# Performance work log

Hardware: AMD Instinct MI355X
Metric: run time of the kernel (lower is better)

Reference implementation:

```python
import jax, jax.numpy as jnp
import numpy as np
from jax import lax

HIDDEN = 1024
OUT = 256
BATCH = 1024
SEQ_LEN = 128


def setup_inputs() -> dict:
    key = jax.random.key(0)
    ks = jax.random.split(key, 7)
    s_ih = 1.0 / np.sqrt(HIDDEN)
    # PyTorch GRUCell params: weight_ih [3H, I], weight_hh [3H, H], biases [3H]
    W_ih = jax.random.uniform(ks[0], (3 * HIDDEN, OUT), jnp.float32, -s_ih, s_ih)
    W_hh = jax.random.uniform(ks[1], (3 * HIDDEN, HIDDEN), jnp.float32, -s_ih, s_ih)
    b_ih = jax.random.uniform(ks[2], (3 * HIDDEN,), jnp.float32, -s_ih, s_ih)
    b_hh = jax.random.uniform(ks[3], (3 * HIDDEN,), jnp.float32, -s_ih, s_ih)
    # xavier_uniform Linear(hidden -> out), bias zero
    lim = float(np.sqrt(2.0) * np.sqrt(6.0 / (HIDDEN + OUT)))
    W_dec = jax.random.uniform(ks[4], (OUT, HIDDEN), jnp.float32, -lim, lim)
    b_dec = jnp.zeros((OUT,), jnp.float32)
    h_0 = jax.random.normal(ks[5], (1, BATCH, HIDDEN), jnp.float32)
    return {
        "h_0": h_0,
        "W_ih": W_ih,
        "W_hh": W_hh,
        "b_ih": b_ih,
        "b_hh": b_hh,
        "W_dec": W_dec,
        "b_dec": b_dec,
        "seq_len": SEQ_LEN,
    }


def _gru_cell(x, h, W_ih, W_hh, b_ih, b_hh):
    # PyTorch GRUCell math
    gi = x @ W_ih.T + b_ih  # [B, 3H]
    gh = h @ W_hh.T + b_hh  # [B, 3H]
    i_r, i_z, i_n = jnp.split(gi, 3, axis=-1)
    h_r, h_z, h_n = jnp.split(gh, 3, axis=-1)
    r = jax.nn.sigmoid(i_r + h_r)
    z = jax.nn.sigmoid(i_z + h_z)
    n = jnp.tanh(i_n + r * h_n)
    return (1.0 - z) * n + z * h


def reference(h_0, W_ih, W_hh, b_ih, b_hh, W_dec, b_dec, seq_len):
    h = h_0[0]  # squeeze(0) -> [B, H]
    x = h @ W_dec.T + b_dec  # initial x_i [B, OUT]

    def step(carry, _):
        h, x = carry
        h_new = _gru_cell(x, h, W_ih, W_hh, b_ih, b_hh)
        x_new = h_new @ W_dec.T + b_dec
        return (h_new, x_new), x_new

    _, xs = lax.scan(step, (h, x), None, length=seq_len)  # [T, B, OUT]
    return jnp.transpose(xs, (1, 0, 2))  # [B, T, OUT]
```

## Files before the change

### kernel.cpp

```cpp
#include <hip/hip_runtime.h>
#include <cstdint>
#include <cstddef>


#define HD 1024
#define OD 256
#define TS 128
#define NBUF 4
#define ABUF 16384
#define BBUF 18432

typedef _Float16 f16x8 __attribute__((ext_vector_type(8)));
typedef float f32x4 __attribute__((ext_vector_type(4)));

template <int AUX>
__device__ __forceinline__ void gl_lds16(const void* g, void* l) {
  auto gp = reinterpret_cast<const __attribute__((address_space(1))) unsigned int*>(
      reinterpret_cast<uintptr_t>(g));
  auto lp = reinterpret_cast<__attribute__((address_space(3))) unsigned int*>(
      reinterpret_cast<uintptr_t>(l));
  __builtin_amdgcn_global_load_lds(gp, lp, 16, 0, AUX);
}

__device__ __forceinline__ void st_h16_dev(_Float16* p, _Float16 v) {
  asm volatile("global_store_short %0, %1, off sc0 sc1"
               :: "v"(p), "v"(v) : "memory");
}

__global__ __launch_bounds__(256) void prep_w(
    const float* __restrict__ Wih,
    const float* __restrict__ Whh,
    const float* __restrict__ Wdec,
    _Float16* __restrict__ Wws)
{
  int blk = blockIdx.x, tid = threadIdx.x;
  int k0 = tid * 4;
  if (blk < 768) {
    int cbv[4], rrv[4], jg[4], jh[4];
    #pragma unroll
    for (int rsel = 0; rsel < 4; ++rsel) {
      int dj = blk * 4 + rsel;
      int cb = dj / 96, rr = dj % 96;
      int s = rr >> 5, wcol = (rr >> 4) & 1, p = rr & 15;
      int j = cb * 32 + wcol * 16 + p;
      cbv[rsel] = cb; rrv[rsel] = rr;
      jg[rsel] = s * 1024 + j;
      jh[rsel] = (s == 0) ? j : (s == 1 ? 1024 + j : -1);
    }
    float acc[4][4];
    #pragma unroll
    for (int a = 0; a < 4; ++a) { acc[a][0]=0.f; acc[a][1]=0.f; acc[a][2]=0.f; acc[a][3]=0.f; }
    for (int q = 0; q < 256; ++q) {
      float4 wd = *(const float4*)(Wdec + (size_t)q * 1024 + k0);
      #pragma unroll
      for (int a = 0; a < 4; ++a) {
        float w = Wih[(size_t)jg[a] * 256 + q];
        acc[a][0] += w * wd.x; acc[a][1] += w * wd.y;
        acc[a][2] += w * wd.z; acc[a][3] += w * wd.w;
      }
    }
    #pragma unroll
    for (int a = 0; a < 4; ++a) {
      if (jh[a] >= 0) {
        const float* wh = Whh + (size_t)jh[a] * 1024 + k0;
        acc[a][0] += wh[0]; acc[a][1] += wh[1];
        acc[a][2] += wh[2]; acc[a][3] += wh[3];
      }
      _Float16* dst = Wws + ((size_t)cbv[a] * 144 + rrv[a]) * 1024 + k0;
      dst[0] = (_Float16)acc[a][0]; dst[1] = (_Float16)acc[a][1];
      dst[2] = (_Float16)acc[a][2]; dst[3] = (_Float16)acc[a][3];
    }
  } else {
    #pragma unroll
    for (int rsel = 0; rsel < 4; ++rsel) {
      int cr = (blk - 768) * 4 + rsel;
      int cb = cr / 48, rr = 96 + cr % 48;
      _Float16* dst = Wws + ((size_t)cb * 144 + rr) * 1024 + k0;
      if (rr < 128) {
        int j = cb * 32 + ((rr >> 4) & 1) * 16 + (rr & 15);
        const float* src = Whh + (size_t)(2048 + j) * 1024 + k0;
        dst[0] = (_Float16)src[0]; dst[1] = (_Float16)src[1];
        dst[2] = (_Float16)src[2]; dst[3] = (_Float16)src[3];
      } else if (rr < 136) {
        const float* src = Wdec + (size_t)(cb * 8 + rr - 128) * 1024 + k0;
        dst[0] = (_Float16)src[0]; dst[1] = (_Float16)src[1];
        dst[2] = (_Float16)src[2]; dst[3] = (_Float16)src[3];
      } else {
        dst[0] = (_Float16)0.f; dst[1] = (_Float16)0.f;
        dst[2] = (_Float16)0.f; dst[3] = (_Float16)0.f;
      }
    }
  }
}

__global__ __launch_bounds__(256) void prep_bias(
    const float* __restrict__ Wih,
    const float* __restrict__ bih, const float* __restrict__ bhh,
    const float* __restrict__ bdec_in,
    float* __restrict__ br, float* __restrict__ bz, float* __restrict__ bin_,
    float* __restrict__ bhn, float* __restrict__ bdec,
    unsigned int* __restrict__ ctr)
{
  int j = blockIdx.x * 256 + threadIdx.x;
  if (blockIdx.x == 0) ctr[threadIdx.x] = 0u;
  float bc0 = 0.f, bc1 = 0.f, bc2 = 0.f;
  for (int q = 0; q < 256; ++q) {
    float bd = bdec_in[q];
    bc0 += Wih[(size_t)j * 256 + q] * bd;
    bc1 += Wih[(size_t)(1024 + j) * 256 + q] * bd;
    bc2 += Wih[(size_t)(2048 + j) * 256 + q] * bd;
  }
  br[j]  = bih[j]        + bhh[j]        + bc0;
  bz[j]  = bih[1024 + j] + bhh[1024 + j] + bc1;
  bin_[j]= bih[2048 + j] + bc2;
  bhn[j] = bhh[2048 + j];
  if (j < 256) bdec[j] = bdec_in[j];
}

__global__ __launch_bounds__(256) void prep_h(
    const float* __restrict__ h0, _Float16* __restrict__ h16)
{
  int i = blockIdx.x * 256 + threadIdx.x;
  h16[i] = (_Float16)h0[i];
}

__global__ __launch_bounds__(256, 1) void fused_gru(
    const _Float16* __restrict__ Wws,
    const float* __restrict__ br, const float* __restrict__ bz,
    const float* __restrict__ bin_, const float* __restrict__ bhn,
    const float* __restrict__ bdec,
    const float* __restrict__ h0,
    _Float16* __restrict__ h16A, _Float16* __restrict__ h16B,
    float* __restrict__ out,
    unsigned int* __restrict__ ctr)
{
  __shared__ __align__(16) char lds[NBUF * (ABUF + BBUF)];

  const int tid = threadIdx.x;
  const int wave = tid >> 6, lane = tid & 63;
  const int mt = blockIdx.x >> 5, cb = blockIdx.x & 31;
  const int wr = wave >> 1, wc = wave & 1;
  const int col16 = lane & 15, quad = lane >> 4;

  const _Float16* __restrict__ slab = Wws + (size_t)cb * (144 * 1024);

  int offs[4];
  #pragma unroll
  for (int jj = 0; jj < 4; ++jj) {
    int m = (wave * 4 + jj) * 64 + lane;
    int r = m >> 3, c = m & 7, g = c ^ (r & 7);
    offs[jj] = r * 1024 + g * 8;
  }
  int offE;
  { int m = 1024 + tid; int r = m >> 3, c = m & 7, g = c ^ (r & 7);
    offE = r * 1024 + g * 8; }

  const int swz = (quad ^ (col16 & 7)) << 4;

  const int j = cb * 32 + wc * 16 + col16;
  const float vbr = br[j], vbz = bz[j], vbi = bin_[j], vbh = bhn[j];
  const float vb = bdec[cb * 8 + (col16 & 7)];

  float hold[4][4];
  #pragma unroll
  for (int fm = 0; fm < 4; ++fm) {
    const int mbase = mt * 128 + 64 * wr + 16 * fm + quad * 4;
    #pragma unroll
    for (int ri = 0; ri < 4; ++ri)
      hold[fm][ri] = h0[(size_t)(mbase + ri) * 1024 + j];
  }
  asm volatile("s_waitcnt vmcnt(0)" ::: "memory");

  auto issue_B = [&](int bsel, int kc) {
    char* Bb = lds + NBUF * ABUF + bsel * BBUF;
    #pragma unroll
    for (int jj = 0; jj < 4; ++jj)
      gl_lds16<0>(slab + offs[jj] + kc, Bb + (wave * 4 + jj) * 1024);
    if (wave < 2)
      gl_lds16<0>(slab + offE + kc, Bb + 16384 + wave * 1024);
  };

  const f32x4 fzero = {0.f, 0.f, 0.f, 0.f};

  issue_B(0, 0);
  issue_B(1, 64);
  issue_B(2, 128);

  #pragma unroll 1
  for (int t = 0; t <= TS; ++t) {
    const _Float16* __restrict__ Abase =
        ((t & 1) ? h16B : h16A) + (size_t)mt * (128 * 1024);
    _Float16* __restrict__ o16 = (t & 1) ? h16A : h16B;

    auto issue_A = [&](int bsel, int kc) {
      char* Ab = lds + bsel * ABUF;
      #pragma unroll
      for (int jj = 0; jj < 4; ++jj)
        gl_lds16<17>(Abase + offs[jj] + kc, Ab + (wave * 4 + jj) * 1024);
    };
    auto issue_set = [&](int bsel, int kc) {
      char* Ab = lds + bsel * ABUF;
      char* Bb = lds + NBUF * ABUF + bsel * BBUF;
      #pragma unroll
      for (int jj = 0; jj < 4; ++jj) {
        gl_lds16<17>(Abase + offs[jj] + kc, Ab + (wave * 4 + jj) * 1024);
        gl_lds16<0>(slab  + offs[jj] + kc, Bb + (wave * 4 + jj) * 1024);
      }
      if (wave < 2)
        gl_lds16<0>(slab + offE + kc, Bb + 16384 + wave * 1024);
    };

    f32x4 accG[4][4]; f32x4 accD[2];
    #pragma unroll
    for (int i = 0; i < 4; ++i)
      #pragma unroll
      for (int jj = 0; jj < 4; ++jj) accG[i][jj] = fzero;
    accD[0] = fzero; accD[1] = fzero;

    issue_A(0, 0);
    issue_A(1, 64);
    issue_A(2, 128);

    #pragma unroll 1
    for (int ki = 0; ki < 16; ++ki) {
      const int cur = ki & 3;
      __builtin_amdgcn_sched_barrier(0);
      if (ki == 0) {
        asm volatile("s_waitcnt vmcnt(8)" ::: "memory");
      } else if (ki == 1) {
        if (wave < 2) asm volatile("s_waitcnt vmcnt(13)" ::: "memory");
        else          asm volatile("s_waitcnt vmcnt(12)" ::: "memory");
      } else if (ki <= 13) {
        if (wave < 2) asm volatile("s_waitcnt vmcnt(18)" ::: "memory");
        else          asm volatile("s_waitcnt vmcnt(16)" ::: "memory");
      } else if (ki == 14) {
        if (wave < 2) asm volatile("s_waitcnt vmcnt(9)" ::: "memory");
        else          asm volatile("s_waitcnt vmcnt(8)" ::: "memory");
      } else {
        asm volatile("s_waitcnt vmcnt(0)" ::: "memory");
      }
      __builtin_amdgcn_s_barrier();
      __builtin_amdgcn_sched_barrier(0);

      if (ki <= 12) issue_set((ki + 3) & 3, (ki + 3) * 64);

      const char* As = lds + cur * ABUF;
      const char* Bs = lds + NBUF * ABUF + cur * BBUF;

      #pragma unroll
      for (int half = 0; half < 2; ++half) {
        const int sz = swz ^ (half << 6);
        f16x8 af[4], bg[4], bdv;
        #pragma unroll
        for (int fm = 0; fm < 4; ++fm)
          af[fm] = *(const f16x8*)(As + (64 * wr + 16 * fm + col16) * 128 + sz);
        #pragma unroll
        for (int fn = 0; fn < 4; ++fn)
          bg[fn] = *(const f16x8*)(Bs + (32 * fn + wc * 16 + col16) * 128 + sz);
        bdv = *(const f16x8*)(Bs + (128 + col16) * 128 + sz);
        const f16x8 adv0 = wc ? af[2] : af[0];
        const f16x8 adv1 = wc ? af[3] : af[1];

        __builtin_amdgcn_s_setprio(1);
        #pragma unroll
        for (int fm = 0; fm < 4; ++fm)
          #pragma unroll
          for (int fn = 0; fn < 4; ++fn)
            accG[fm][fn] = __builtin_amdgcn_mfma_f32_16x16x32_f16(af[fm], bg[fn], accG[fm][fn], 0, 0, 0);
        accD[0] = __builtin_amdgcn_mfma_f32_16x16x32_f16(adv0, bdv, accD[0], 0, 0, 0);
        accD[1] = __builtin_amdgcn_mfma_f32_16x16x32_f16(adv1, bdv, accD[1], 0, 0, 0);
        __builtin_amdgcn_s_setprio(0);
      }
    }

    if (t < TS) {
      #pragma unroll
      for (int fm = 0; fm < 4; ++fm) {
        const int mbase = mt * 128 + 64 * wr + 16 * fm + quad * 4;
        #pragma unroll
        for (int ri = 0; ri < 4; ++ri) {
          const int m = mbase + ri;
          float rg = 1.f / (1.f + __expf(-(accG[fm][0][ri] + vbr)));
          float zg = 1.f / (1.f + __expf(-(accG[fm][1][ri] + vbz)));
          float nn = tanhf(accG[fm][2][ri] + vbi + rg * (accG[fm][3][ri] + vbh));
          float hnew = (1.f - zg) * nn + zg * hold[fm][ri];
          hold[fm][ri] = hnew;
          st_h16_dev(o16 + (size_t)m * 1024 + j, (_Float16)hnew);
        }
      }
    }
    if (t > 0 && col16 < 8) {
      const int oc = cb * 8 + col16;
      #pragma unroll
      for (int d = 0; d < 2; ++d) {
        const int mbase = mt * 128 + 32 * wave + 16 * d + quad * 4;
        #pragma unroll
        for (int ri = 0; ri < 4; ++ri) {
          const int m = mbase + ri;
          out[(size_t)m * (TS * OD) + (size_t)(t - 1) * OD + oc] = accD[d][ri] + vb;
        }
      }
    }

    if (t < TS) {
      __syncthreads();
      issue_B(0, 0);
      issue_B(1, 64);
      issue_B(2, 128);
      if (tid == 0) {
        __hip_atomic_fetch_add(&ctr[mt * 32], 1u, __ATOMIC_RELAXED, __HIP_MEMORY_SCOPE_AGENT);
        while (__hip_atomic_load(&ctr[mt * 32], __ATOMIC_RELAXED, __HIP_MEMORY_SCOPE_AGENT)
               < 32u * (unsigned)(t + 1)) {
          __builtin_amdgcn_s_sleep(1);
        }
      }
      __builtin_amdgcn_s_barrier();
      __builtin_amdgcn_sched_barrier(0);
    }
  }
}

__global__ __launch_bounds__(256, 1) void step_kernel(
    const _Float16* __restrict__ Wws,
    const float* __restrict__ br, const float* __restrict__ bz,
    const float* __restrict__ bin_, const float* __restrict__ bhn,
    const float* __restrict__ bdec,
    const _Float16* __restrict__ h_in16, const float* __restrict__ h_in32,
    _Float16* __restrict__ h_out16, float* __restrict__ h_out32,
    float* __restrict__ out, int t)
{
  __shared__ __align__(16) char lds[2 * 16384 + 2 * 18432];

  const int tid = threadIdx.x;
  const int wave = tid >> 6, lane = tid & 63;
  const int mt = blockIdx.x >> 5, cb = blockIdx.x & 31;
  const int wr = wave >> 1, wc = wave & 1;
  const int col16 = lane & 15, quad = lane >> 4;

  const _Float16* __restrict__ slab  = Wws + (size_t)cb * (144 * 1024);
  const _Float16* __restrict__ Abase = h_in16 + (size_t)mt * (128 * 1024);

  int offs[4];
  #pragma unroll
  for (int jj = 0; jj < 4; ++jj) {
    int m = (wave * 4 + jj) * 64 + lane;
    int r = m >> 3, c = m & 7, g = c ^ (r & 7);
    offs[jj] = r * 1024 + g * 8;
  }
  int offE;
  { int m = 1024 + tid; int r = m >> 3, c = m & 7, g = c ^ (r & 7);
    offE = r * 1024 + g * 8; }

  const int swz = (quad ^ (col16 & 7)) << 4;

  f32x4 accG[4][4]; f32x4 accD[2];
  const f32x4 fzero = {0.f, 0.f, 0.f, 0.f};
  #pragma unroll
  for (int i = 0; i < 4; ++i)
    #pragma unroll
    for (int jj = 0; jj < 4; ++jj) accG[i][jj] = fzero;
  accD[0] = fzero; accD[1] = fzero;

  auto issue_dma = [&](int bsel, int kc) {
    char* Ab = lds + bsel * 16384;
    char* Bb = lds + 32768 + bsel * 18432;
    #pragma unroll
    for (int jj = 0; jj < 4; ++jj) {
      gl_lds16<0>(Abase + offs[jj] + kc, Ab + (wave * 4 + jj) * 1024);
      gl_lds16<0>(slab  + offs[jj] + kc, Bb + (wave * 4 + jj) * 1024);
    }
    if (wave < 2)
      gl_lds16<0>(slab + offE + kc, Bb + 16384 + wave * 1024);
  };

  issue_dma(0, 0);
  __syncthreads();

  #pragma unroll 1
  for (int ki = 0; ki < 16; ++ki) {
    const int cur = ki & 1;
    if (ki < 15) issue_dma(cur ^ 1, (ki + 1) * 64);
    const char* As = lds + cur * 16384;
    const char* Bs = lds + 32768 + cur * 18432;

    #pragma unroll
    for (int half = 0; half < 2; ++half) {
      const int sz = swz ^ (half << 6);
      f16x8 af[4], bg[4], bdv;
      #pragma unroll
      for (int fm = 0; fm < 4; ++fm)
        af[fm] = *(const f16x8*)(As + (64 * wr + 16 * fm + col16) * 128 + sz);
      #pragma unroll
      for (int fn = 0; fn < 4; ++fn)
        bg[fn] = *(const f16x8*)(Bs + (32 * fn + wc * 16 + col16) * 128 + sz);
      bdv = *(const f16x8*)(Bs + (128 + col16) * 128 + sz);
      const f16x8 adv0 = wc ? af[2] : af[0];
      const f16x8 adv1 = wc ? af[3] : af[1];

      #pragma unroll
      for (int fm = 0; fm < 4; ++fm)
        #pragma unroll
        for (int fn = 0; fn < 4; ++fn)
          accG[fm][fn] = __builtin_amdgcn_mfma_f32_16x16x32_f16(af[fm], bg[fn], accG[fm][fn], 0, 0, 0);
      accD[0] = __builtin_amdgcn_mfma_f32_16x16x32_f16(adv0, bdv, accD[0], 0, 0, 0);
      accD[1] = __builtin_amdgcn_mfma_f32_16x16x32_f16(adv1, bdv, accD[1], 0, 0, 0);
    }
    __syncthreads();
  }

  if (t < TS) {
    const int jj2 = cb * 32 + wc * 16 + col16;
    const float vbr = br[jj2], vbz = bz[jj2], vbi = bin_[jj2], vbh = bhn[jj2];
    #pragma unroll
    for (int fm = 0; fm < 4; ++fm) {
      const int mbase = mt * 128 + 64 * wr + 16 * fm + quad * 4;
      #pragma unroll
      for (int ri = 0; ri < 4; ++ri) {
        const int m = mbase + ri;
        float rg = 1.f / (1.f + __expf(-(accG[fm][0][ri] + vbr)));
        float zg = 1.f / (1.f + __expf(-(accG[fm][1][ri] + vbz)));
        float nn = tanhf(accG[fm][2][ri] + vbi + rg * (accG[fm][3][ri] + vbh));
        float hold = h_in32[(size_t)m * 1024 + jj2];
        float hnew = (1.f - zg) * nn + zg * hold;
        h_out32[(size_t)m * 1024 + jj2] = hnew;
        h_out16[(size_t)m * 1024 + jj2] = (_Float16)hnew;
      }
    }
  }
  if (t > 0 && col16 < 8) {
    const int oc = cb * 8 + col16;
    const float vb = bdec[oc];
    #pragma unroll
    for (int d = 0; d < 2; ++d) {
      const int mbase = mt * 128 + 32 * wave + 16 * d + quad * 4;
      #pragma unroll
      for (int ri = 0; ri < 4; ++ri) {
        const int m = mbase + ri;
        out[(size_t)m * (TS * OD) + (size_t)(t - 1) * OD + oc] = accD[d][ri] + vb;
      }
    }
  }
}

extern "C" void kernel_launch(void* const* d_in, const int* in_sizes, int n_in,
                              void* d_out, int out_size, void* d_ws, size_t ws_size,
                              hipStream_t stream) {
  const float* h0      = (const float*)d_in[0];
  const float* Wih     = (const float*)d_in[1];
  const float* Whh     = (const float*)d_in[2];
  const float* bih     = (const float*)d_in[3];
  const float* bhh     = (const float*)d_in[4];
  const float* Wdec    = (const float*)d_in[5];
  const float* bdec_in = (const float*)d_in[6];
  float* out = (float*)d_out;

  char* ws = (char*)d_ws;
  _Float16* Wws = (_Float16*)ws;
  float* br   = (float*)(ws + 9437184);
  float* bz   = (float*)(ws + 9437184 + 4096);
  float* bin_ = (float*)(ws + 9437184 + 8192);
  float* bhn  = (float*)(ws + 9437184 + 12288);
  float* bdec = (float*)(ws + 9437184 + 16384);
  _Float16* h16A = (_Float16*)(ws + 9461760);
  _Float16* h16B = h16A + 1024 * 1024;
  unsigned int* ctr = (unsigned int*)(ws + 9461760 + 4194304);
  float* h32A = (float*)(ws + 9461760 + 4194304 + 4096);
  float* h32B = h32A + 1024 * 1024;

  prep_w<<<1152, 256, 0, stream>>>(Wih, Whh, Wdec, Wws);
  prep_bias<<<4, 256, 0, stream>>>(Wih, bih, bhh, bdec_in, br, bz, bin_, bhn, bdec, ctr);
  prep_h<<<4096, 256, 0, stream>>>(h0, h16A);

  void* kargs[] = {
    (void*)&Wws, (void*)&br, (void*)&bz, (void*)&bin_, (void*)&bhn, (void*)&bdec,
    (void*)&h0, (void*)&h16A, (void*)&h16B, (void*)&out, (void*)&ctr
  };
  hipError_t cerr = hipLaunchCooperativeKernel((void*)fused_gru, dim3(256), dim3(256),
                                               kargs, 0, stream);
  if (cerr != hipSuccess) {
    for (int t = 0; t <= TS; ++t) {
      const _Float16* in16 = (t & 1) ? h16B : h16A;
      const float*    in32 = (t == 0) ? h0 : ((t & 1) ? h32B : h32A);
      _Float16*       o16  = (t & 1) ? h16A : h16B;
      float*          o32  = (t & 1) ? h32A : h32B;
      step_kernel<<<256, 256, 0, stream>>>(Wws, br, bz, bin_, bhn, bdec,
                                           in16, in32, o16, o32, out, t);
    }
  }
}
```

Measured before the change: 2.582 ms.

## Split K across two wave groups in fused GRU kernel with LDS reduction

Doubles the persistent block to 512 threads: two groups of four waves each compute half of the K dimension, each with its own double-buffered A/B staging, and then exchange partial accumulators through LDS to reduce before the gate epilogue. Each group handles half of the epilogue rows, and the weight prefetch for the next step is issued before the epilogue. The intent is more waves per CU to hide load latency on the latency-bound recurrent step, at the cost of an extra LDS reduction, extra barriers, and a shallower pipeline (2 buffers per group instead of 4). tanhf is also replaced with an exp-based fast tanh.

```diff
diff --git a/kernel.cpp b/kernel.cpp
--- a/kernel.cpp
+++ b/kernel.cpp
@@ -6,7 +6,6 @@
 #define HD 1024
 #define OD 256
 #define TS 128
-#define NBUF 4
 #define ABUF 16384
 #define BBUF 18432
 
@@ -25,6 +24,10 @@
 __device__ __forceinline__ void st_h16_dev(_Float16* p, _Float16 v) {
   asm volatile("global_store_short %0, %1, off sc0 sc1"
                :: "v"(p), "v"(v) : "memory");
+}
+
+__device__ __forceinline__ float fast_tanh(float x) {
+  return 1.f - 2.f / (__expf(2.f * x) + 1.f);
 }
 
 __global__ __launch_bounds__(256) void prep_w(
@@ -124,7 +127,7 @@
   h16[i] = (_Float16)h0[i];
 }
 
-__global__ __launch_bounds__(256, 1) void fused_gru(
+__global__ __launch_bounds__(512, 2) void fused_gru(
     const _Float16* __restrict__ Wws,
     const float* __restrict__ br, const float* __restrict__ bz,
     const float* __restrict__ bin_, const float* __restrict__ bhn,
@@ -134,12 +137,13 @@
     float* __restrict__ out,
     unsigned int* __restrict__ ctr)
 {
-  __shared__ __align__(16) char lds[NBUF * (ABUF + BBUF)];
+  __shared__ __align__(16) char lds[4 * (ABUF + BBUF) + 8192];
 
   const int tid = threadIdx.x;
   const int wave = tid >> 6, lane = tid & 63;
+  const int s = wave >> 2, p = wave & 3;
   const int mt = blockIdx.x >> 5, cb = blockIdx.x & 31;
-  const int wr = wave >> 1, wc = wave & 1;
+  const int wr = p >> 1, wc = p & 1;
   const int col16 = lane & 15, quad = lane >> 4;
 
   const _Float16* __restrict__ slab = Wws + (size_t)cb * (144 * 1024);
@@ -147,12 +151,12 @@
   int offs[4];
   #pragma unroll
   for (int jj = 0; jj < 4; ++jj) {
-    int m = (wave * 4 + jj) * 64 + lane;
+    int m = (p * 4 + jj) * 64 + lane;
     int r = m >> 3, c = m & 7, g = c ^ (r & 7);
     offs[jj] = r * 1024 + g * 8;
   }
   int offE;
-  { int m = 1024 + tid; int r = m >> 3, c = m & 7, g = c ^ (r & 7);
+  { int m = 1024 + (p * 64 + lane); int r = m >> 3, c = m & 7, g = c ^ (r & 7);
     offE = r * 1024 + g * 8; }
 
   const int swz = (quad ^ (col16 & 7)) << 4;
@@ -161,30 +165,31 @@
   const float vbr = br[j], vbz = bz[j], vbi = bin_[j], vbh = bhn[j];
   const float vb = bdec[cb * 8 + (col16 & 7)];
 
-  float hold[4][4];
+  float hold[2][4];
   #pragma unroll
-  for (int fm = 0; fm < 4; ++fm) {
+  for (int f2 = 0; f2 < 2; ++f2) {
+    const int fm = 2 * s + f2;
     const int mbase = mt * 128 + 64 * wr + 16 * fm + quad * 4;
     #pragma unroll
     for (int ri = 0; ri < 4; ++ri)
-      hold[fm][ri] = h0[(size_t)(mbase + ri) * 1024 + j];
+      hold[f2][ri] = h0[(size_t)(mbase + ri) * 1024 + j];
   }
   asm volatile("s_waitcnt vmcnt(0)" ::: "memory");
 
-  auto issue_B = [&](int bsel, int kc) {
-    char* Bb = lds + NBUF * ABUF + bsel * BBUF;
+  auto issue_B = [&](int i, int ki) {
+    char* Bb = lds + 4 * ABUF + (s * 2 + i) * BBUF;
+    const int kc = (s * 8 + ki) * 64;
     #pragma unroll
     for (int jj = 0; jj < 4; ++jj)
-      gl_lds16<0>(slab + offs[jj] + kc, Bb + (wave * 4 + jj) * 1024);
-    if (wave < 2)
-      gl_lds16<0>(slab + offE + kc, Bb + 16384 + wave * 1024);
+      gl_lds16<0>(slab + offs[jj] + kc, Bb + (p * 4 + jj) * 1024);
+    if (p < 2)
+      gl_lds16<0>(slab + offE + kc, Bb + 16384 + p * 1024);
   };
 
   const f32x4 fzero = {0.f, 0.f, 0.f, 0.f};
 
   issue_B(0, 0);
-  issue_B(1, 64);
-  issue_B(2, 128);
+  issue_B(1, 1);
 
   #pragma unroll 1
   for (int t = 0; t <= TS; ++t) {
@@ -192,22 +197,24 @@
         ((t & 1) ? h16B : h16A) + (size_t)mt * (128 * 1024);
     _Float16* __restrict__ o16 = (t & 1) ? h16A : h16B;
 
-    auto issue_A = [&](int bsel, int kc) {
-      char* Ab = lds + bsel * ABUF;
+    auto issue_A = [&](int i, int ki) {
+      char* Ab = lds + (s * 2 + i) * ABUF;
+      const int kc = (s * 8 + ki) * 64;
       #pragma unroll
       for (int jj = 0; jj < 4; ++jj)
-        gl_lds16<17>(Abase + offs[jj] + kc, Ab + (wave * 4 + jj) * 1024);
+        gl_lds16<17>(Abase + offs[jj] + kc, Ab + (p * 4 + jj) * 1024);
     };
-    auto issue_set = [&](int bsel, int kc) {
-      char* Ab = lds + bsel * ABUF;
-      char* Bb = lds + NBUF * ABUF + bsel * BBUF;
+    auto issue_set = [&](int i, int ki) {
+      char* Ab = lds + (s * 2 + i) * ABUF;
+      char* Bb = lds + 4 * ABUF + (s * 2 + i) * BBUF;
+      const int kc = (s * 8 + ki) * 64;
       #pragma unroll
       for (int jj = 0; jj < 4; ++jj) {
-        gl_lds16<17>(Abase + offs[jj] + kc, Ab + (wave * 4 + jj) * 1024);
-        gl_lds16<0>(slab  + offs[jj] + kc, Bb + (wave * 4 + jj) * 1024);
-      }
-      if (wave < 2)
-        gl_lds16<0>(slab + offE + kc, Bb + 16384 + wave * 1024);
+        gl_lds16<17>(Abase + offs[jj] + kc, Ab + (p * 4 + jj) * 1024);
+        gl_lds16<0>(slab  + offs[jj] + kc, Bb + (p * 4 + jj) * 1024);
+      }
+      if (p < 2)
+        gl_lds16<0>(slab + offE + kc, Bb + 16384 + p * 1024);
     };
 
     f32x4 accG[4][4]; f32x4 accD[2];
@@ -218,34 +225,25 @@
     accD[0] = fzero; accD[1] = fzero;
 
     issue_A(0, 0);
-    issue_A(1, 64);
-    issue_A(2, 128);
+    issue_A(1, 1);
 
     #pragma unroll 1
-    for (int ki = 0; ki < 16; ++ki) {
-      const int cur = ki & 3;
+    for (int ki = 0; ki < 8; ++ki) {
+      const int cur = ki & 1;
       __builtin_amdgcn_sched_barrier(0);
       if (ki == 0) {
-        asm volatile("s_waitcnt vmcnt(8)" ::: "memory");
-      } else if (ki == 1) {
-        if (wave < 2) asm volatile("s_waitcnt vmcnt(13)" ::: "memory");
-        else          asm volatile("s_waitcnt vmcnt(12)" ::: "memory");
-      } else if (ki <= 13) {
-        if (wave < 2) asm volatile("s_waitcnt vmcnt(18)" ::: "memory");
-        else          asm volatile("s_waitcnt vmcnt(16)" ::: "memory");
-      } else if (ki == 14) {
-        if (wave < 2) asm volatile("s_waitcnt vmcnt(9)" ::: "memory");
-        else          asm volatile("s_waitcnt vmcnt(8)" ::: "memory");
+        asm volatile("s_waitcnt vmcnt(4)" ::: "memory");
+      } else if (ki < 7) {
+        if (p < 2) asm volatile("s_waitcnt vmcnt(9)" ::: "memory");
+        else       asm volatile("s_waitcnt vmcnt(8)" ::: "memory");
       } else {
         asm volatile("s_waitcnt vmcnt(0)" ::: "memory");
       }
       __builtin_amdgcn_s_barrier();
       __builtin_amdgcn_sched_barrier(0);
 
-      if (ki <= 12) issue_set((ki + 3) & 3, (ki + 3) * 64);
-
-      const char* As = lds + cur * ABUF;
-      const char* Bs = lds + NBUF * ABUF + cur * BBUF;
+      const char* As = lds + (s * 2 + cur) * ABUF;
+      const char* Bs = lds + 4 * ABUF + (s * 2 + cur) * BBUF;
 
       #pragma unroll
       for (int half = 0; half < 2; ++half) {
@@ -271,29 +269,72 @@
         accD[1] = __builtin_amdgcn_mfma_f32_16x16x32_f16(adv1, bdv, accD[1], 0, 0, 0);
         __builtin_amdgcn_s_setprio(0);
       }
-    }
+
+      __builtin_amdgcn_sched_barrier(0);
+      __builtin_amdgcn_s_barrier();
+      __builtin_amdgcn_sched_barrier(0);
+      if (ki <= 5) issue_set(cur, ki + 2);
+    }
+
+    __syncthreads();
+    {
+      char* Xg = lds + (size_t)((s * 4 + p) * 64 + lane) * 128;
+      #pragma unroll
+      for (int f2 = 0; f2 < 2; ++f2)
+        #pragma unroll
+        for (int fn = 0; fn < 4; ++fn) {
+          f32x4 v = s ? accG[f2][fn] : accG[2 + f2][fn];
+          *(f32x4*)(Xg + (f2 * 4 + fn) * 16) = v;
+        }
+      if (s == 1) {
+        char* Xd = lds + 4 * (ABUF + BBUF) + (size_t)(p * 64 + lane) * 32;
+        *(f32x4*)(Xd)      = accD[0];
+        *(f32x4*)(Xd + 16) = accD[1];
+      }
+    }
+    __syncthreads();
+    f32x4 accK[2][4];
+    {
+      const char* Xg = lds + (size_t)(((1 - s) * 4 + p) * 64 + lane) * 128;
+      #pragma unroll
+      for (int f2 = 0; f2 < 2; ++f2)
+        #pragma unroll
+        for (int fn = 0; fn < 4; ++fn) {
+          f32x4 mine = s ? accG[2 + f2][fn] : accG[f2][fn];
+          f32x4 oth = *(const f32x4*)(Xg + (f2 * 4 + fn) * 16);
+          accK[f2][fn] = mine + oth;
+        }
+      if (s == 0) {
+        const char* Xd = lds + 4 * (ABUF + BBUF) + (size_t)(p * 64 + lane) * 32;
+        accD[0] += *(const f32x4*)(Xd);
+        accD[1] += *(const f32x4*)(Xd + 16);
+      }
+    }
+
+    if (t < TS) { issue_B(0, 0); issue_B(1, 1); }
 
     if (t < TS) {
       #pragma unroll
-      for (int fm = 0; fm < 4; ++fm) {
+      for (int f2 = 0; f2 < 2; ++f2) {
+        const int fm = 2 * s + f2;
         const int mbase = mt * 128 + 64 * wr + 16 * fm + quad * 4;
         #pragma unroll
         for (int ri = 0; ri < 4; ++ri) {
           const int m = mbase + ri;
-          float rg = 1.f / (1.f + __expf(-(accG[fm][0][ri] + vbr)));
-          float zg = 1.f / (1.f + __expf(-(accG[fm][1][ri] + vbz)));
-          float nn = tanhf(accG[fm][2][ri] + vbi + rg * (accG[fm][3][ri] + vbh));
-          float hnew = (1.f - zg) * nn + zg * hold[fm][ri];
-          hold[fm][ri] = hnew;
+          float rg = 1.f / (1.f + __expf(-(accK[f2][0][ri] + vbr)));
+          float zg = 1.f / (1.f + __expf(-(accK[f2][1][ri] + vbz)));
+          float nn = fast_tanh(accK[f2][2][ri] + vbi + rg * (accK[f2][3][ri] + vbh));
+          float hnew = (1.f - zg) * nn + zg * hold[f2][ri];
+          hold[f2][ri] = hnew;
           st_h16_dev(o16 + (size_t)m * 1024 + j, (_Float16)hnew);
         }
       }
     }
-    if (t > 0 && col16 < 8) {
+    if (t > 0 && s == 0 && col16 < 8) {
       const int oc = cb * 8 + col16;
       #pragma unroll
       for (int d = 0; d < 2; ++d) {
-        const int mbase = mt * 128 + 32 * wave + 16 * d + quad * 4;
+        const int mbase = mt * 128 + 32 * p + 16 * d + quad * 4;
         #pragma unroll
         for (int ri = 0; ri < 4; ++ri) {
           const int m = mbase + ri;
@@ -304,9 +345,6 @@
 
     if (t < TS) {
       __syncthreads();
-      issue_B(0, 0);
-      issue_B(1, 64);
-      issue_B(2, 128);
       if (tid == 0) {
         __hip_atomic_fetch_add(&ctr[mt * 32], 1u, __ATOMIC_RELAXED, __HIP_MEMORY_SCOPE_AGENT);
         while (__hip_atomic_load(&ctr[mt * 32], __ATOMIC_RELAXED, __HIP_MEMORY_SCOPE_AGENT)
@@ -419,7 +457,7 @@
         const int m = mbase + ri;
         float rg = 1.f / (1.f + __expf(-(accG[fm][0][ri] + vbr)));
         float zg = 1.f / (1.f + __expf(-(accG[fm][1][ri] + vbz)));
-        float nn = tanhf(accG[fm][2][ri] + vbi + rg * (accG[fm][3][ri] + vbh));
+        float nn = fast_tanh(accG[fm][2][ri] + vbi + rg * (accG[fm][3][ri] + vbh));
         float hold = h_in32[(size_t)m * 1024 + jj2];
         float hnew = (1.f - zg) * nn + zg * hold;
         h_out32[(size_t)m * 1024 + jj2] = hnew;
@@ -475,7 +513,7 @@
     (void*)&Wws, (void*)&br, (void*)&bz, (void*)&bin_, (void*)&bhn, (void*)&bdec,
     (void*)&h0, (void*)&h16A, (void*)&h16B, (void*)&out, (void*)&ctr
   };
-  hipError_t cerr = hipLaunchCooperativeKernel((void*)fused_gru, dim3(256), dim3(256),
+  hipError_t cerr = hipLaunchCooperativeKernel((void*)fused_gru, dim3(256), dim3(512),
                                                kargs, 0, stream);
   if (cerr != hipSuccess) {
     for (int t = 0; t <= TS; ++t) {
```

Result: faster. 2.376 ms (-8.0%).
